# Kernel tuning notes

Hardware: AMD Instinct MI355X
Metric: run time of the kernel (lower is better)

The kernel has to match this reference:

```python
import jax, jax.numpy as jnp
import numpy as np

N = 131072          # batch of (action, condition) pairs
ACT_D = 12          # action_dim
COND_D = 256        # condition_dim
K = 256             # num_embeddings (codebook size)
E = 16              # embedding_dim
H1, H2 = 512, 256   # encoder_hidden_dims
COMMIT = 0.25       # commitment_cost
EPS_NORM = 1e-12    # F.normalize eps


def _normalize(x):
    n = jnp.linalg.norm(x, axis=-1, keepdims=True)
    return x / jnp.maximum(n, EPS_NORM)


def setup_inputs() -> dict:
    key = jax.random.key(0)
    ks = jax.random.split(key, 16)
    s = 0.02
    return {
        "actions": jax.random.normal(ks[0], (N, ACT_D), jnp.float32),
        "conditions": jax.random.normal(ks[1], (N, COND_D), jnp.float32),
        # encoder: (COND_D+ACT_D) -> H1 -> H2 -> E  (weights stored [in, out])
        "enc_w1": jax.random.normal(ks[2], (COND_D + ACT_D, H1), jnp.float32) * s,
        "enc_b1": jnp.zeros((H1,), jnp.float32),
        "enc_w2": jax.random.normal(ks[3], (H1, H2), jnp.float32) * s,
        "enc_b2": jnp.zeros((H2,), jnp.float32),
        "enc_w3": jax.random.normal(ks[4], (H2, E), jnp.float32) * s,
        "enc_b3": jnp.zeros((E,), jnp.float32),
        # decoder: (COND_D+E) -> H2 -> H1 -> ACT_D
        "dec_w1": jax.random.normal(ks[5], (COND_D + E, H2), jnp.float32) * s,
        "dec_b1": jnp.zeros((H2,), jnp.float32),
        "dec_w2": jax.random.normal(ks[6], (H2, H1), jnp.float32) * s,
        "dec_b2": jnp.zeros((H1,), jnp.float32),
        "dec_w3": jax.random.normal(ks[7], (H1, ACT_D), jnp.float32) * s,
        "dec_b3": jnp.zeros((ACT_D,), jnp.float32),
        # codebook, init U(-1/K, 1/K) like nn.Embedding in the module
        "embedding": jax.random.uniform(ks[8], (K, E), jnp.float32, -1.0 / K, 1.0 / K),
    }


def reference(actions, conditions, enc_w1, enc_b1, enc_w2, enc_b2, enc_w3, enc_b3,
              dec_w1, dec_b1, dec_w2, dec_b2, dec_w3, dec_b3, embedding):
    sg = jax.lax.stop_gradient
    elu = jax.nn.elu

    # ---- encoder ----
    x = jnp.concatenate([actions, conditions], axis=-1)          # [N, ACT_D+COND_D]
    h = elu(x @ enc_w1 + enc_b1)
    h = elu(h @ enc_w2 + enc_b2)
    z = h @ enc_w3 + enc_b3                                      # [N, E]

    # ---- vector quantizer (distance='cos') ----
    normed_in = sg(_normalize(z))                                # inputs.detach()
    normed_w = _normalize(embedding)
    distances = normed_in @ normed_w.T                           # [N, K] cosine sims

    idx = jnp.argmax(distances, axis=-1)                         # [N]
    quantized = embedding[idx]                                   # one-hot @ codebook == gather

    e_latent_loss = COMMIT * jnp.mean((sg(quantized) - z) ** 2)
    q_latent_loss = jnp.mean((quantized - sg(z)) ** 2)
    quantized_st = z + sg(quantized - z)                         # straight-through

    counts = jnp.zeros((K,), distances.dtype).at[idx].add(1.0)
    avg_probs = counts / N                                       # mean of one-hot encodings
    perplexity = jnp.exp(-jnp.sum(avg_probs * jnp.log(avg_probs + 1e-10)))

    # ---- contrastive loss (training branch, deterministic part) ----
    sortd = jnp.sort(distances, axis=0)                          # ascending per codeword
    n_pos = max(1, N // K)
    dis_pos = jnp.mean(sortd[-n_pos:, :], axis=0, keepdims=True) # [1, K] hardest positives
    dis_neg = sortd[: N // 2, :]                                 # [N//2, K]
    dis = jnp.concatenate([dis_pos, dis_neg], axis=0).T / 0.07   # [K, 1+N//2]
    # cross-entropy with target class 0
    contra_loss = jnp.mean(jax.nn.logsumexp(dis, axis=1) - dis[:, 0])

    # ---- decoder ----
    d = jnp.concatenate([quantized_st, conditions], axis=-1)     # [N, E+COND_D]
    d = elu(d @ dec_w1 + dec_b1)
    d = elu(d @ dec_w2 + dec_b2)
    reconstructed = d @ dec_w3 + dec_b3                          # [N, ACT_D]

    reconstruction_loss = jnp.mean((reconstructed - actions) ** 2)

    return (reconstructed, quantized_st, idx.astype(jnp.int32), q_latent_loss,
            e_latent_loss, contra_loss, perplexity, reconstruction_loss)
```

## Files before the change

### kernel.cpp

```cpp
#include <hip/hip_runtime.h>
#include <hip/hip_bf16.h>
#include <math.h>

#define NROWS 131072
#define ACT_D 12
#define COND_D 256
#define KEMB 256
#define EDIM 16
#define H1D 512
#define H2D 256
#define NB 16384

typedef __attribute__((ext_vector_type(8))) _Float16 half8;
typedef __attribute__((ext_vector_type(4))) float floatx4;
typedef unsigned short ushort_t;

#define LO_SCALE 4096.0f
#define INV_LO_SCALE 2.44140625e-4f


__global__ void init_kernel(int* counts, float* outScal) {
    int t = threadIdx.x;
    counts[t] = 0;
    if (t < 5) outScal[t] = 0.0f;
}

__device__ inline ushort_t f16bits(_Float16 h) { return __builtin_bit_cast(ushort_t, h); }
__device__ inline float f16pair(ushort_t a, ushort_t b) {
    return (float)__builtin_bit_cast(_Float16, a)
         + (float)__builtin_bit_cast(_Float16, b) * INV_LO_SCALE;
}
__device__ inline void splitf(float v, ushort_t& hi, ushort_t& lo) {
    _Float16 h = (_Float16)v;
    _Float16 l = (_Float16)((v - (float)h) * LO_SCALE);
    hi = f16bits(h); lo = f16bits(l);
}

__device__ inline void gload_lds16(const void* g, void* lds) {
    __builtin_amdgcn_global_load_lds((const __attribute__((address_space(1))) void*)g,
                                     (__attribute__((address_space(3))) void*)lds, 16, 0, 0);
}

__global__ __launch_bounds__(256)
void convw_kernel(const float* __restrict__ W, ushort_t* __restrict__ Whi,
                  ushort_t* __restrict__ Wlo, int K, int N, int Kp)
{
    int n = blockIdx.x;
    int k = blockIdx.y * 256 + threadIdx.x;
    if (k >= Kp) return;
    float v = (k < K) ? W[(long)k * N + n] : 0.0f;
    ushort_t h, l; splitf(v, h, l);
    Whi[(long)n * Kp + k] = h;
    Wlo[(long)n * Kp + k] = l;
}

template<int CONCAT>
__global__ __launch_bounds__(256, 3)
void gemm_f16x3_kernel(const void* A0v, const void* A1v,
                       const ushort_t* __restrict__ Bhi, const ushort_t* __restrict__ Blo,
                       const float* __restrict__ bias,
                       ushort_t* __restrict__ Chi, ushort_t* __restrict__ Clo,
                       int Nw, int Kp, int Kvalid)
{
    __shared__ uint lds[12288];
    const int tid = threadIdx.x;
    const int w = tid >> 6, l = tid & 63;
    const int quad = l >> 4, lr = l & 15;
    const long rowBase = (long)blockIdx.x * 64;
    const int colBase = blockIdx.y * 128;
    const int nQ = w * 32;

    floatx4 accH[4][2], accX[4][2];
#pragma unroll
    for (int i = 0; i < 4; ++i)
#pragma unroll
        for (int j = 0; j < 2; ++j) { accH[i][j] = (floatx4)(0.0f); accX[i][j] = (floatx4)(0.0f); }

    const ushort_t* pBh0 = Bhi + (long)(colBase + l) * Kp + w * 8;
    const ushort_t* pBh1 = pBh0 + (long)64 * Kp;
    const ushort_t* pBl0 = Blo + (long)(colBase + l) * Kp + w * 8;
    const ushort_t* pBl1 = pBl0 + (long)64 * Kp;

    auto stageB = [&](int buf, int k0) {
        uint* d = &lds[buf * 6144 + 2048 + w * 512];
        gload_lds16(pBh0 + k0, d);
        gload_lds16(pBh1 + k0, d + 256);
        gload_lds16(pBl0 + k0, d + 2048);
        gload_lds16(pBl1 + k0, d + 2048 + 256);
    };

    const ushort_t* pAh = (const ushort_t*)A0v + (rowBase + l) * Kp + w * 8;
    const ushort_t* pAl = (const ushort_t*)A1v + (rowBase + l) * Kp + w * 8;
    auto stageA0 = [&](int buf, int k0) {
        uint* d = &lds[buf * 6144 + w * 256];
        gload_lds16(pAh + k0, d);
        gload_lds16(pAl + k0, d + 1024);
    };

    const float* A1p = (const float*)A0v;
    const float* A2p = (const float*)A1v;
    const long grow = rowBase + l;

    auto aload = [&](float* v, int k0) -> bool {
        const int kk = k0 + w * 8;
        if (kk >= CONCAT && kk + 8 <= Kvalid) {
            const float* p = A2p + grow * COND_D + (kk - CONCAT);
            *(float4*)&v[0] = *(const float4*)p;
            *(float4*)&v[4] = *(const float4*)(p + 4);
            return true;
        } else if (kk + 8 <= CONCAT) {
            const float* p = A1p + grow * CONCAT + kk;
            *(float4*)&v[0] = *(const float4*)p;
            *(float4*)&v[4] = *(const float4*)(p + 4);
            return true;
        } else {
#pragma unroll
            for (int i = 0; i < 8; ++i) {
                int k = kk + i;
                v[i] = (k < CONCAT) ? A1p[grow * CONCAT + k]
                     : (k < Kvalid) ? A2p[grow * COND_D + (k - CONCAT)] : 0.0f;
            }
            return false;
        }
    };
    auto awrite = [&](int buf, const float* v) {
        uint hh[4], ll[4];
#pragma unroll
        for (int i = 0; i < 4; ++i) {
            ushort_t h0, l0, h1, l1;
            splitf(v[2 * i], h0, l0);
            splitf(v[2 * i + 1], h1, l1);
            hh[i] = (uint)h0 | ((uint)h1 << 16);
            ll[i] = (uint)l0 | ((uint)l1 << 16);
        }
        *(uint4*)&lds[buf * 6144 + w * 256 + l * 4]        = *(uint4*)hh;
        *(uint4*)&lds[buf * 6144 + 1024 + w * 256 + l * 4] = *(uint4*)ll;
    };

    auto compute = [&](int buf) {
        const int base = buf * 6144;
        half8 bh[2], bl[2];
#pragma unroll
        for (int jn = 0; jn < 2; ++jn) {
            int boff = base + 2048 + quad * 512 + (nQ + jn * 16 + lr) * 4;
            bh[jn] = __builtin_bit_cast(half8, *(uint4*)&lds[boff]);
            bl[jn] = __builtin_bit_cast(half8, *(uint4*)&lds[boff + 2048]);
        }
#pragma unroll
        for (int im = 0; im < 4; ++im) {
            int aoff = base + quad * 256 + (im * 16 + lr) * 4;
            half8 ah = __builtin_bit_cast(half8, *(uint4*)&lds[aoff]);
            half8 al = __builtin_bit_cast(half8, *(uint4*)&lds[aoff + 1024]);
#pragma unroll
            for (int jn = 0; jn < 2; ++jn) {
                accH[im][jn] = __builtin_amdgcn_mfma_f32_16x16x32_f16(ah, bh[jn], accH[im][jn], 0, 0, 0);
                accX[im][jn] = __builtin_amdgcn_mfma_f32_16x16x32_f16(ah, bl[jn], accX[im][jn], 0, 0, 0);
                accX[im][jn] = __builtin_amdgcn_mfma_f32_16x16x32_f16(al, bh[jn], accX[im][jn], 0, 0, 0);
            }
        }
    };

    const int kTiles = Kp / 32;
    int cur = 0;
    float v[8];
    bool fast = true;
    (void)fast;

    if constexpr (CONCAT == 0) {
        stageB(0, 0);
        stageA0(0, 0);
    } else {
        fast = aload(v, 0);
        stageB(0, 0);
        awrite(0, v);
        asm volatile("s_waitcnt lgkmcnt(0)" ::: "memory");
        __builtin_amdgcn_sched_barrier(0);
    }

    for (int t = 0; t < kTiles - 1; ++t) {
        const int k0n = (t + 1) * 32;
        if constexpr (CONCAT == 0) {
            stageB(cur ^ 1, k0n);
            stageA0(cur ^ 1, k0n);
            asm volatile("s_waitcnt vmcnt(6)" ::: "memory");
            __builtin_amdgcn_sched_barrier(0);
        } else {
            fast = aload(v, k0n);
            stageB(cur ^ 1, k0n);
            if (fast) asm volatile("s_waitcnt vmcnt(6)" ::: "memory");
            else      asm volatile("s_waitcnt vmcnt(4)" ::: "memory");
            __builtin_amdgcn_sched_barrier(0);
        }
        __builtin_amdgcn_s_barrier();
        __builtin_amdgcn_s_setprio(1);
        compute(cur);
        __builtin_amdgcn_s_setprio(0);
        if constexpr (CONCAT != 0) {
            awrite(cur ^ 1, v);
            asm volatile("s_waitcnt lgkmcnt(0)" ::: "memory");
            __builtin_amdgcn_sched_barrier(0);
        }
        __builtin_amdgcn_s_barrier();
        cur ^= 1;
    }
    asm volatile("s_waitcnt vmcnt(0)" ::: "memory");
    __builtin_amdgcn_sched_barrier(0);
    __builtin_amdgcn_s_barrier();
    compute(cur);

    float bv[2];
#pragma unroll
    for (int jn = 0; jn < 2; ++jn) bv[jn] = bias[colBase + nQ + jn * 16 + lr];
#pragma unroll
    for (int im = 0; im < 4; ++im) {
#pragma unroll
        for (int jn = 0; jn < 2; ++jn) {
            int n = colBase + nQ + jn * 16 + lr;
#pragma unroll
            for (int rr = 0; rr < 4; ++rr) {
                long m = rowBase + im * 16 + quad * 4 + rr;
                float x = accH[im][jn][rr] + accX[im][jn][rr] * INV_LO_SCALE + bv[jn];
                x = x > 0.0f ? x : (expf(x) - 1.0f);
                ushort_t h, lo; splitf(x, h, lo);
                long idx = m * Nw + n;
                Chi[idx] = h;
                Clo[idx] = lo;
            }
        }
    }
}

__global__ __launch_bounds__(256)
void quantize_kernel(const ushort_t* __restrict__ h2hi, const ushort_t* __restrict__ h2lo,
                     const float* __restrict__ W3,
                     const float* __restrict__ b3, const float* __restrict__ emb,
                     float* __restrict__ distT, float* __restrict__ outQ,
                     float* __restrict__ outIdx, int* __restrict__ counts,
                     float* __restrict__ qsum)
{
    __shared__ float h2t[16 * 260];
    __shared__ float w3t[16 * 260];
    __shared__ float nwt[256 * 20];
    __shared__ float zt[16 * 17];
    __shared__ float dt[16 * 257];
    __shared__ int   lcnt[256];
    __shared__ float swred[4];

    int t = threadIdx.x;
    long rowBase = (long)blockIdx.x * 16;

    for (int it = 0; it < 16; ++it) {
        long idx = (rowBase + it) * 256 + t;
        h2t[it * 260 + t] = f16pair(h2hi[idx], h2lo[idx]);
    }
    for (int it = 0; it < 16; ++it) {
        int flat = it * 256 + t;
        int j = flat >> 4, c = flat & 15;
        w3t[c * 260 + j] = W3[flat];
    }
    {
        float e0[16]; float ss = 0.f;
#pragma unroll
        for (int i = 0; i < 16; ++i) { e0[i] = emb[t * 16 + i]; ss += e0[i] * e0[i]; }
        float inv = 1.0f / fmaxf(sqrtf(ss), 1e-12f);
#pragma unroll
        for (int i = 0; i < 16; ++i) nwt[t * 20 + i] = e0[i] * inv;
    }
    lcnt[t] = 0;
    __syncthreads();

    int r = t >> 4, c = t & 15;
    float zacc = b3[c];
    for (int j4 = 0; j4 < 64; ++j4) {
        float4 h = *(const float4*)&h2t[r * 260 + j4 * 4];
        float4 w = *(const float4*)&w3t[c * 260 + j4 * 4];
        zacc += h.x * w.x + h.y * w.y + h.z * w.z + h.w * w.w;
    }
    float ss = zacc * zacc;
#pragma unroll
    for (int m = 1; m < 16; m <<= 1) ss += __shfl_xor(ss, m, 64);
    zt[r * 17 + c] = zacc / fmaxf(sqrtf(ss), 1e-12f);
    __syncthreads();

    float zr[16];
#pragma unroll
    for (int e = 0; e < 16; ++e) zr[e] = zt[r * 17 + e];
    float best = -1e30f; int bidx = 0;
    for (int cc = 0; cc < 16; ++cc) {
        int col = cc * 16 + c;
        float d = 0.f;
#pragma unroll
        for (int e4 = 0; e4 < 4; ++e4) {
            float4 wv = *(const float4*)&nwt[col * 20 + e4 * 4];
            d += zr[e4 * 4 + 0] * wv.x + zr[e4 * 4 + 1] * wv.y
               + zr[e4 * 4 + 2] * wv.z + zr[e4 * 4 + 3] * wv.w;
        }
        dt[r * 257 + col] = d;
        if (d > best || (d == best && col < bidx)) { best = d; bidx = col; }
    }
#pragma unroll
    for (int m = 1; m < 16; m <<= 1) {
        float ov = __shfl_xor(best, m, 64);
        int   oi = __shfl_xor(bidx, m, 64);
        if (ov > best || (ov == best && oi < bidx)) { best = ov; bidx = oi; }
    }

    float q = emb[bidx * 16 + c];
    outQ[(rowBase + r) * 16 + c] = q;
    float df = q - zacc;
    float part = df * df;
#pragma unroll
    for (int m = 1; m < 64; m <<= 1) part += __shfl_xor(part, m, 64);
    if ((t & 63) == 0) swred[t >> 6] = part;
    if (c == 0) {
        outIdx[rowBase + r] = (float)bidx;
        atomicAdd(&lcnt[bidx], 1);
    }
    __syncthreads();
    if (t == 0) atomicAdd(qsum, swred[0] + swred[1] + swred[2] + swred[3]);
    if (lcnt[t] > 0) atomicAdd(&counts[t], lcnt[t]);

    int rr = t & 15, cg = t >> 4;
    for (int i = 0; i < 16; ++i) {
        int col = i * 16 + cg;
        distT[(long)col * NROWS + rowBase + rr] = dt[rr * 257 + col];
    }
}

__global__ __launch_bounds__(1024)
void selA_kernel(const float* __restrict__ distT, int* __restrict__ stats)
{
    __shared__ int hist[NB];
    __shared__ int part[1024];
    int t = threadIdx.x, c = blockIdx.x;
    for (int i = t; i < NB; i += 1024) hist[i] = 0;
    __syncthreads();
    const float* col = distT + (long)c * NROWS;
    for (int i = t; i < NROWS; i += 1024) {
        float v = col[i];
        int b = (int)((v + 1.0f) * (NB * 0.5f));
        b = min(max(b, 0), NB - 1);
        atomicAdd(&hist[b], 1);
    }
    __syncthreads();
    const int CH = NB / 1024;
    int s = 0;
    for (int i = 0; i < CH; ++i) s += hist[t * CH + i];
    part[t] = s;
    __syncthreads();
    if (t == 0) {
        int target = NROWS / 2;
        int cum = 0; int chunk = 0;
        while (cum + part[chunk] < target) { cum += part[chunk]; ++chunk; }
        int b = chunk * CH;
        while (cum + hist[b] < target) { cum += hist[b]; ++b; }
        int medBin = b, needLow = target - cum, cntMed = hist[b];
        int cumA = 0; chunk = 1023;
        while (cumA + part[chunk] < 512) { cumA += part[chunk]; --chunk; }
        b = chunk * CH + CH - 1;
        while (cumA + hist[b] < 512) { cumA += hist[b]; --b; }
        int topBin = b, needTop = 512 - cumA, cntTop = hist[b];
        int* st = stats + c * 6;
        st[0] = medBin; st[1] = needLow; st[2] = cntMed;
        st[3] = topBin; st[4] = needTop; st[5] = cntTop;
    }
}

__global__ __launch_bounds__(1024)
void selB_kernel(const float* __restrict__ distT, const int* __restrict__ stats,
                 float* __restrict__ contra_sum)
{
    __shared__ float red[64];
    int t = threadIdx.x, c = blockIdx.x;
    const int* st = stats + c * 6;
    int medBin = st[0], needLow = st[1], cntMed = st[2];
    int topBin = st[3], needTop = st[4], cntTop = st[5];
    const float binw = 2.0f / NB;
    float mUp = -1.0f + (medBin + 1) * binw;
    const float INVT = 1.0f / 0.07f;
    const float* col = distT + (long)c * NROWS;
    float topS = 0.f, tbS = 0.f, lowS = 0.f, mbS = 0.f;
    for (int i = t; i < NROWS; i += 1024) {
        float v = col[i];
        int b = (int)((v + 1.0f) * (NB * 0.5f));
        b = min(max(b, 0), NB - 1);
        if (b > topBin)       topS += v;
        else if (b == topBin) tbS += v;
        if (b < medBin)       lowS += expf((v - mUp) * INVT);
        else if (b == medBin) mbS  += expf((v - mUp) * INVT);
    }
#pragma unroll
    for (int m = 1; m < 64; m <<= 1) {
        topS += __shfl_xor(topS, m, 64);
        tbS  += __shfl_xor(tbS, m, 64);
        lowS += __shfl_xor(lowS, m, 64);
        mbS  += __shfl_xor(mbS, m, 64);
    }
    if ((t & 63) == 0) {
        int wv = t >> 6;
        red[wv * 4 + 0] = topS; red[wv * 4 + 1] = tbS;
        red[wv * 4 + 2] = lowS; red[wv * 4 + 3] = mbS;
    }
    __syncthreads();
    if (t == 0) {
        float T0 = 0, T1 = 0, T2 = 0, T3 = 0;
        for (int wv = 0; wv < 16; ++wv) {
            T0 += red[wv * 4 + 0]; T1 += red[wv * 4 + 1];
            T2 += red[wv * 4 + 2]; T3 += red[wv * 4 + 3];
        }
        float dis_pos = (T0 + needTop * (T1 / cntTop)) * (1.0f / 512.0f);
        float S = T2 + needLow * (T3 / cntMed);
        float colContra = log1pf(S * expf((mUp - dis_pos) * INVT));
        atomicAdd(contra_sum, colContra);
    }
}

__global__ __launch_bounds__(256)
void dec3_kernel(const ushort_t* __restrict__ d2hi, const ushort_t* __restrict__ d2lo,
                 const float* __restrict__ W,
                 const float* __restrict__ bias, const float* __restrict__ actions,
                 float* __restrict__ rec, float* __restrict__ recon_sum)
{
    __shared__ float dtile[16 * 516];
    __shared__ float wt[512 * 12];
    __shared__ float red2[4];
    int t = threadIdx.x;
    long rowBase = (long)blockIdx.x * 16;
    for (int it = 0; it < 24; ++it) wt[it * 256 + t] = W[it * 256 + t];
    for (int it = 0; it < 32; ++it) {
        int flat = it * 256 + t;
        int r = flat >> 9, k = flat & 511;
        long idx = (rowBase + r) * 512 + k;
        dtile[r * 516 + k] = f16pair(d2hi[idx], d2lo[idx]);
    }
    __syncthreads();
    float part = 0.f;
    if (t < 192) {
        int r = t / 12, cc = t % 12;
        float acc = bias[cc];
        for (int k4 = 0; k4 < 128; ++k4) {
            float4 h = *(const float4*)&dtile[r * 516 + k4 * 4];
            acc += h.x * wt[(k4 * 4 + 0) * 12 + cc] + h.y * wt[(k4 * 4 + 1) * 12 + cc]
                 + h.z * wt[(k4 * 4 + 2) * 12 + cc] + h.w * wt[(k4 * 4 + 3) * 12 + cc];
        }
        rec[(rowBase + r) * 12 + cc] = acc;
        float df = acc - actions[(rowBase + r) * 12 + cc];
        part = df * df;
    }
#pragma unroll
    for (int m = 1; m < 64; m <<= 1) part += __shfl_xor(part, m, 64);
    if ((t & 63) == 0) red2[t >> 6] = part;
    __syncthreads();
    if (t == 0) atomicAdd(recon_sum, red2[0] + red2[1] + red2[2] + red2[3]);
}

__global__ void finalize_kernel(const int* __restrict__ counts, float* __restrict__ outScal)
{
    __shared__ float red[4];
    int t = threadIdx.x;
    float p = counts[t] * (1.0f / NROWS);
    float term = p * logf(p + 1e-10f);
#pragma unroll
    for (int m = 1; m < 64; m <<= 1) term += __shfl_xor(term, m, 64);
    if ((t & 63) == 0) red[t >> 6] = term;
    __syncthreads();
    if (t == 0) {
        float hsum = red[0] + red[1] + red[2] + red[3];
        float qsum = outScal[0], contra = outScal[2], recon = outScal[4];
        float ql = qsum * (1.0f / (NROWS * 16.0f));
        outScal[0] = ql;
        outScal[1] = 0.25f * ql;
        outScal[2] = contra * (1.0f / 256.0f);
        outScal[3] = expf(-hsum);
        outScal[4] = recon * (1.0f / (NROWS * 12.0f));
    }
}

extern "C" void kernel_launch(void* const* d_in, const int* in_sizes, int n_in,
                              void* d_out, int out_size, void* d_ws, size_t ws_size,
                              hipStream_t stream)
{
    const float* actions    = (const float*)d_in[0];
    const float* conditions = (const float*)d_in[1];
    const float* enc_w1 = (const float*)d_in[2];
    const float* enc_b1 = (const float*)d_in[3];
    const float* enc_w2 = (const float*)d_in[4];
    const float* enc_b2 = (const float*)d_in[5];
    const float* enc_w3 = (const float*)d_in[6];
    const float* enc_b3 = (const float*)d_in[7];
    const float* dec_w1 = (const float*)d_in[8];
    const float* dec_b1 = (const float*)d_in[9];
    const float* dec_w2 = (const float*)d_in[10];
    const float* dec_b2 = (const float*)d_in[11];
    const float* dec_w3 = (const float*)d_in[12];
    const float* dec_b3 = (const float*)d_in[13];
    const float* emb    = (const float*)d_in[14];

    float* out     = (float*)d_out;
    float* outRec  = out;
    float* outQ    = out + (long)NROWS * 12;
    float* outIdx  = out + (long)NROWS * 28;
    float* outScal = out + (long)NROWS * 29;

    ushort_t* wb    = (ushort_t*)d_out;
    ushort_t* w1hi  = wb;            ushort_t* w1lo  = wb + 147456;
    ushort_t* w2hi  = wb + 294912;   ushort_t* w2lo  = wb + 425984;
    ushort_t* wd1hi = wb + 557056;   ushort_t* wd1lo = wb + 630784;
    ushort_t* wd2hi = wb + 704512;   ushort_t* wd2lo = wb + 835584;

    float* ws = (float*)d_ws;
    int* counts = (int*)ws;
    int* stats  = (int*)(ws + 256);
    ushort_t* h2hi = (ushort_t*)(ws + 1792);
    ushort_t* h2lo = (ushort_t*)(ws + 16779008);
    ushort_t* d1hi = h2hi;
    ushort_t* d1lo = h2lo;
    float*    P1   = ws + 33556224;
    ushort_t* h1hi = (ushort_t*)P1;
    ushort_t* h1lo = (ushort_t*)(ws + 67110656);
    float*    distT = P1;
    ushort_t* d2hi = h1hi;
    ushort_t* d2lo = h1lo;

    hipLaunchKernelGGL(init_kernel, dim3(1), dim3(256), 0, stream, counts, outScal);
    hipLaunchKernelGGL(convw_kernel, dim3(512, 2), dim3(256), 0, stream, enc_w1, w1hi, w1lo, 268, 512, 288);
    hipLaunchKernelGGL(convw_kernel, dim3(256, 2), dim3(256), 0, stream, enc_w2, w2hi, w2lo, 512, 256, 512);
    hipLaunchKernelGGL(convw_kernel, dim3(256, 2), dim3(256), 0, stream, dec_w1, wd1hi, wd1lo, 272, 256, 288);
    hipLaunchKernelGGL(convw_kernel, dim3(512, 1), dim3(256), 0, stream, dec_w2, wd2hi, wd2lo, 256, 512, 256);
    hipLaunchKernelGGL((gemm_f16x3_kernel<ACT_D>), dim3(2048, 4), dim3(256), 0, stream,
                       (const void*)actions, (const void*)conditions, w1hi, w1lo, enc_b1,
                       h1hi, h1lo, H1D, 288, 268);
    hipLaunchKernelGGL((gemm_f16x3_kernel<0>), dim3(2048, 2), dim3(256), 0, stream,
                       (const void*)h1hi, (const void*)h1lo, w2hi, w2lo, enc_b2,
                       h2hi, h2lo, H2D, 512, 512);
    hipLaunchKernelGGL(quantize_kernel, dim3(8192), dim3(256), 0, stream,
                       h2hi, h2lo, enc_w3, enc_b3, emb, distT, outQ, outIdx, counts, &outScal[0]);
    hipLaunchKernelGGL(selA_kernel, dim3(256), dim3(1024), 0, stream, distT, stats);
    hipLaunchKernelGGL(selB_kernel, dim3(256), dim3(1024), 0, stream, distT, stats, &outScal[2]);
    hipLaunchKernelGGL((gemm_f16x3_kernel<EDIM>), dim3(2048, 2), dim3(256), 0, stream,
                       (const void*)outQ, (const void*)conditions, wd1hi, wd1lo, dec_b1,
                       d1hi, d1lo, H2D, 288, 272);
    hipLaunchKernelGGL((gemm_f16x3_kernel<0>), dim3(2048, 4), dim3(256), 0, stream,
                       (const void*)d1hi, (const void*)d1lo, wd2hi, wd2lo, dec_b2,
                       d2hi, d2lo, H1D, 256, 256);
    hipLaunchKernelGGL(dec3_kernel, dim3(8192), dim3(256), 0, stream,
                       d2hi, d2lo, dec_w3, dec_b3, actions, outRec, &outScal[4]);
    hipLaunchKernelGGL(finalize_kernel, dim3(1), dim3(256), 0, stream, counts, outScal);
}
```

Baseline: 1.583 ms.

## Load B fragments directly into registers instead of staging through LDS

The GEMM kernel stops staging B (weight hi/lo) tiles through shared memory. Each lane now loads its MFMA B fragments straight from global memory into registers, which shrinks LDS from 48KB to 16KB per block. The hand-tuned vmcnt waits, sched barriers and setprio are replaced by a simpler loop with __syncthreads and a prefetch of the next B tile after compute. This frees LDS for occupancy and removes LDS traffic for B. In exchange, B loads are no longer shared across the block, so global and L2 traffic rises, and the software pipelining is less precisely controlled.

```diff
diff --git a/kernel.cpp b/kernel.cpp
--- a/kernel.cpp
+++ b/kernel.cpp
@@ -62,7 +62,7 @@
                        ushort_t* __restrict__ Chi, ushort_t* __restrict__ Clo,
                        int Nw, int Kp, int Kvalid)
 {
-    __shared__ uint lds[12288];
+    __shared__ uint lds[4096];
     const int tid = threadIdx.x;
     const int w = tid >> 6, l = tid & 63;
     const int quad = l >> 4, lr = l & 15;
@@ -76,23 +76,24 @@
 #pragma unroll
         for (int j = 0; j < 2; ++j) { accH[i][j] = (floatx4)(0.0f); accX[i][j] = (floatx4)(0.0f); }
 
-    const ushort_t* pBh0 = Bhi + (long)(colBase + l) * Kp + w * 8;
-    const ushort_t* pBh1 = pBh0 + (long)64 * Kp;
-    const ushort_t* pBl0 = Blo + (long)(colBase + l) * Kp + w * 8;
-    const ushort_t* pBl1 = pBl0 + (long)64 * Kp;
-
-    auto stageB = [&](int buf, int k0) {
-        uint* d = &lds[buf * 6144 + 2048 + w * 512];
-        gload_lds16(pBh0 + k0, d);
-        gload_lds16(pBh1 + k0, d + 256);
-        gload_lds16(pBl0 + k0, d + 2048);
-        gload_lds16(pBl1 + k0, d + 2048 + 256);
+    const long nIdx0 = colBase + nQ + lr;
+    const ushort_t* pF0h = Bhi + nIdx0 * Kp + quad * 8;
+    const ushort_t* pF1h = pF0h + 16 * Kp;
+    const ushort_t* pF0l = Blo + nIdx0 * Kp + quad * 8;
+    const ushort_t* pF1l = pF0l + 16 * Kp;
+
+    uint4 bch0, bch1, bcl0, bcl1;
+    auto loadB = [&](int k0) {
+        bch0 = *(const uint4*)(pF0h + k0);
+        bch1 = *(const uint4*)(pF1h + k0);
+        bcl0 = *(const uint4*)(pF0l + k0);
+        bcl1 = *(const uint4*)(pF1l + k0);
     };
 
     const ushort_t* pAh = (const ushort_t*)A0v + (rowBase + l) * Kp + w * 8;
     const ushort_t* pAl = (const ushort_t*)A1v + (rowBase + l) * Kp + w * 8;
     auto stageA0 = [&](int buf, int k0) {
-        uint* d = &lds[buf * 6144 + w * 256];
+        uint* d = &lds[buf * 2048 + w * 256];
         gload_lds16(pAh + k0, d);
         gload_lds16(pAl + k0, d + 1024);
     };
@@ -101,18 +102,16 @@
     const float* A2p = (const float*)A1v;
     const long grow = rowBase + l;
 
-    auto aload = [&](float* v, int k0) -> bool {
+    auto aload = [&](float* v, int k0) {
         const int kk = k0 + w * 8;
         if (kk >= CONCAT && kk + 8 <= Kvalid) {
             const float* p = A2p + grow * COND_D + (kk - CONCAT);
             *(float4*)&v[0] = *(const float4*)p;
             *(float4*)&v[4] = *(const float4*)(p + 4);
-            return true;
         } else if (kk + 8 <= CONCAT) {
             const float* p = A1p + grow * CONCAT + kk;
             *(float4*)&v[0] = *(const float4*)p;
             *(float4*)&v[4] = *(const float4*)(p + 4);
-            return true;
         } else {
 #pragma unroll
             for (int i = 0; i < 8; ++i) {
@@ -120,7 +119,6 @@
                 v[i] = (k < CONCAT) ? A1p[grow * CONCAT + k]
                      : (k < Kvalid) ? A2p[grow * COND_D + (k - CONCAT)] : 0.0f;
             }
-            return false;
         }
     };
     auto awrite = [&](int buf, const float* v) {
@@ -133,80 +131,63 @@
             hh[i] = (uint)h0 | ((uint)h1 << 16);
             ll[i] = (uint)l0 | ((uint)l1 << 16);
         }
-        *(uint4*)&lds[buf * 6144 + w * 256 + l * 4]        = *(uint4*)hh;
-        *(uint4*)&lds[buf * 6144 + 1024 + w * 256 + l * 4] = *(uint4*)ll;
+        *(uint4*)&lds[buf * 2048 + w * 256 + l * 4]        = *(uint4*)hh;
+        *(uint4*)&lds[buf * 2048 + 1024 + w * 256 + l * 4] = *(uint4*)ll;
     };
 
     auto compute = [&](int buf) {
-        const int base = buf * 6144;
-        half8 bh[2], bl[2];
-#pragma unroll
-        for (int jn = 0; jn < 2; ++jn) {
-            int boff = base + 2048 + quad * 512 + (nQ + jn * 16 + lr) * 4;
-            bh[jn] = __builtin_bit_cast(half8, *(uint4*)&lds[boff]);
-            bl[jn] = __builtin_bit_cast(half8, *(uint4*)&lds[boff + 2048]);
-        }
+        const int base = buf * 2048;
+        half8 bh0 = __builtin_bit_cast(half8, bch0);
+        half8 bh1 = __builtin_bit_cast(half8, bch1);
+        half8 bl0 = __builtin_bit_cast(half8, bcl0);
+        half8 bl1 = __builtin_bit_cast(half8, bcl1);
 #pragma unroll
         for (int im = 0; im < 4; ++im) {
             int aoff = base + quad * 256 + (im * 16 + lr) * 4;
             half8 ah = __builtin_bit_cast(half8, *(uint4*)&lds[aoff]);
             half8 al = __builtin_bit_cast(half8, *(uint4*)&lds[aoff + 1024]);
-#pragma unroll
-            for (int jn = 0; jn < 2; ++jn) {
-                accH[im][jn] = __builtin_amdgcn_mfma_f32_16x16x32_f16(ah, bh[jn], accH[im][jn], 0, 0, 0);
-                accX[im][jn] = __builtin_amdgcn_mfma_f32_16x16x32_f16(ah, bl[jn], accX[im][jn], 0, 0, 0);
-                accX[im][jn] = __builtin_amdgcn_mfma_f32_16x16x32_f16(al, bh[jn], accX[im][jn], 0, 0, 0);
-            }
+            accH[im][0] = __builtin_amdgcn_mfma_f32_16x16x32_f16(ah, bh0, accH[im][0], 0, 0, 0);
+            accX[im][0] = __builtin_amdgcn_mfma_f32_16x16x32_f16(ah, bl0, accX[im][0], 0, 0, 0);
+            accX[im][0] = __builtin_amdgcn_mfma_f32_16x16x32_f16(al, bh0, accX[im][0], 0, 0, 0);
+            accH[im][1] = __builtin_amdgcn_mfma_f32_16x16x32_f16(ah, bh1, accH[im][1], 0, 0, 0);
+            accX[im][1] = __builtin_amdgcn_mfma_f32_16x16x32_f16(ah, bl1, accX[im][1], 0, 0, 0);
+            accX[im][1] = __builtin_amdgcn_mfma_f32_16x16x32_f16(al, bh1, accX[im][1], 0, 0, 0);
         }
     };
 
     const int kTiles = Kp / 32;
     int cur = 0;
     float v[8];
-    bool fast = true;
-    (void)fast;
 
     if constexpr (CONCAT == 0) {
-        stageB(0, 0);
         stageA0(0, 0);
+        loadB(0);
+        __syncthreads();
     } else {
-        fast = aload(v, 0);
-        stageB(0, 0);
+        aload(v, 0);
+        loadB(0);
         awrite(0, v);
-        asm volatile("s_waitcnt lgkmcnt(0)" ::: "memory");
-        __builtin_amdgcn_sched_barrier(0);
-    }
-
-    for (int t = 0; t < kTiles - 1; ++t) {
+        __syncthreads();
+    }
+
+    for (int t = 0; t < kTiles; ++t) {
+        const bool hasNext = (t + 1 < kTiles);
         const int k0n = (t + 1) * 32;
         if constexpr (CONCAT == 0) {
-            stageB(cur ^ 1, k0n);
-            stageA0(cur ^ 1, k0n);
-            asm volatile("s_waitcnt vmcnt(6)" ::: "memory");
-            __builtin_amdgcn_sched_barrier(0);
+            if (hasNext) stageA0(cur ^ 1, k0n);
+            compute(cur);
+            if (hasNext) loadB(k0n);
         } else {
-            fast = aload(v, k0n);
-            stageB(cur ^ 1, k0n);
-            if (fast) asm volatile("s_waitcnt vmcnt(6)" ::: "memory");
-            else      asm volatile("s_waitcnt vmcnt(4)" ::: "memory");
-            __builtin_amdgcn_sched_barrier(0);
-        }
-        __builtin_amdgcn_s_barrier();
-        __builtin_amdgcn_s_setprio(1);
-        compute(cur);
-        __builtin_amdgcn_s_setprio(0);
-        if constexpr (CONCAT != 0) {
-            awrite(cur ^ 1, v);
-            asm volatile("s_waitcnt lgkmcnt(0)" ::: "memory");
-            __builtin_amdgcn_sched_barrier(0);
-        }
-        __builtin_amdgcn_s_barrier();
+            if (hasNext) aload(v, k0n);
+            compute(cur);
+            if (hasNext) {
+                awrite(cur ^ 1, v);
+                loadB(k0n);
+            }
+        }
+        __syncthreads();
         cur ^= 1;
     }
-    asm volatile("s_waitcnt vmcnt(0)" ::: "memory");
-    __builtin_amdgcn_sched_barrier(0);
-    __builtin_amdgcn_s_barrier();
-    compute(cur);
 
     float bv[2];
 #pragma unroll
```

After: 1.470 ms. 7.2% less time.
